# Kernel optimization log

Measured on AMD Instinct MI355X. Metric: run time of the kernel, lower is better.

The kernel has to match this reference:

```python
import jax, jax.numpy as jnp
import numpy as np

N_NODES = 500000
N_EDGES = 8000000


def gcn_conv(x, W, b, src, dst, n_nodes):
    # PyG GCNConv: add self-loops, symmetric normalization, x@W, scatter-add.
    loop = jnp.arange(n_nodes, dtype=src.dtype)
    src_a = jnp.concatenate([src, loop])  # [E+N]
    dst_a = jnp.concatenate([dst, loop])
    deg = jax.ops.segment_sum(jnp.ones_like(dst_a, dtype=x.dtype), dst_a,
                              num_segments=n_nodes)  # in-degree incl. self-loop
    dinv = jnp.where(deg > 0, jax.lax.rsqrt(deg), 0.0)
    norm = dinv[src_a] * dinv[dst_a]  # [E+N]
    xw = x @ W  # [N, out]
    msg = xw[src_a] * norm[:, None]  # [E+N, out]
    out = jax.ops.segment_sum(msg, dst_a, num_segments=n_nodes)
    return out + b


def setup_inputs() -> dict:
    key = jax.random.key(0)
    k1, k2, k3, k4, k5, k6 = jax.random.split(key, 6)
    x = jax.random.uniform(k1, (N_NODES, 1), dtype=jnp.float32)
    edge_index = jax.random.randint(k2, (2, N_EDGES), 0, N_NODES, dtype=jnp.int32)
    W1 = jax.random.normal(k3, (1, 16), dtype=jnp.float32)
    b1 = jax.random.normal(k4, (16,), dtype=jnp.float32) * 0.1
    W2 = jax.random.normal(k5, (16, 2), dtype=jnp.float32)
    b2 = jax.random.normal(k6, (2,), dtype=jnp.float32) * 0.1
    return {"x": x, "edge_index": edge_index, "W1": W1, "b1": b1,
            "W2": W2, "b2": b2}


def reference(x, edge_index, W1, b1, W2, b2):
    src, dst = edge_index[0], edge_index[1]
    h = gcn_conv(x, W1, b1, src, dst, N_NODES)
    h = jax.nn.relu(h)
    # dropout is identity in eval mode
    h = gcn_conv(h, W2, b2, src, dst, N_NODES)
    return jax.nn.log_softmax(h, axis=1)
```

## Files before the change

### kernel.cpp

```cpp
#include <hip/hip_runtime.h>
#include <math.h>


typedef unsigned int uint4v __attribute__((ext_vector_type(4)));

#define NPB 1024
#define NPB_SHIFT 10
#define NPB_MASK (NPB - 1)
#define MAXB 512
#define P1T 512
#define CHUNK 16384
#define SORT_CAP 17408
#define SPT 17

__device__ __forceinline__ unsigned short f2bf(float f) {
    unsigned int x = __float_as_uint(f);
    x += 0x7fffu + ((x >> 16) & 1u);
    return (unsigned short)(x >> 16);
}
__device__ __forceinline__ float bf2f(unsigned short h) {
    return __uint_as_float((unsigned int)h << 16);
}

__global__ __launch_bounds__(P1T, 4) void k_bucket(
    const int* __restrict__ src, const int* __restrict__ dst,
    unsigned int* __restrict__ file, int* __restrict__ ctr,
    int E, int nbucket, int cap)
{
    __shared__ unsigned int sorted[CHUNK];
    __shared__ int cnt[MAXB];
    __shared__ int pre[MAXB + 1];
    __shared__ int gb[MAXB];
    __shared__ int rk[MAXB];

    const int t  = threadIdx.x;
    const int e0 = blockIdx.x * CHUNK;
    const int nE = min(CHUNK, E - e0);

    for (int b = t; b < MAXB; b += P1T) { cnt[b] = 0; rk[b] = 0; }
    __syncthreads();

    const bool full = (nE == CHUNK);
    int4 dc[8];

    if (full) {
        const int4* d4 = (const int4*)(dst + e0);
#pragma unroll
        for (int k = 0; k < 8; ++k) dc[k] = d4[t + k * P1T];
#pragma unroll
        for (int k = 0; k < 8; ++k) {
            atomicAdd(&cnt[((unsigned)dc[k].x) >> NPB_SHIFT], 1);
            atomicAdd(&cnt[((unsigned)dc[k].y) >> NPB_SHIFT], 1);
            atomicAdd(&cnt[((unsigned)dc[k].z) >> NPB_SHIFT], 1);
            atomicAdd(&cnt[((unsigned)dc[k].w) >> NPB_SHIFT], 1);
        }
    } else {
        for (int i = t; i < nE; i += P1T)
            atomicAdd(&cnt[((unsigned)dst[e0 + i]) >> NPB_SHIFT], 1);
    }
    __syncthreads();

    int v = (t < nbucket) ? cnt[t] : 0;
    pre[t + 1] = v;
    if (t == 0) pre[0] = 0;
    __syncthreads();
    for (int off = 1; off < P1T; off <<= 1) {
        int add = (t >= off) ? pre[t + 1 - off] : 0;
        __syncthreads();
        pre[t + 1] += add;
        __syncthreads();
    }

    for (int b = t; b < nbucket; b += P1T) {
        int c = cnt[b];
        gb[b] = c ? atomicAdd(&ctr[b], c) : 0;
    }
    __syncthreads();

    if (full) {
        const int4* s4 = (const int4*)(src + e0);
#pragma unroll
        for (int k = 0; k < 8; ++k) {
            int4 s = s4[t + k * P1T];
            int4 d = dc[k];
            {
                int b = ((unsigned)d.x) >> NPB_SHIFT;
                int r = atomicAdd(&rk[b], 1);
                sorted[pre[b] + r] = (((unsigned)s.x) << NPB_SHIFT) | ((unsigned)d.x & NPB_MASK);
            }
            {
                int b = ((unsigned)d.y) >> NPB_SHIFT;
                int r = atomicAdd(&rk[b], 1);
                sorted[pre[b] + r] = (((unsigned)s.y) << NPB_SHIFT) | ((unsigned)d.y & NPB_MASK);
            }
            {
                int b = ((unsigned)d.z) >> NPB_SHIFT;
                int r = atomicAdd(&rk[b], 1);
                sorted[pre[b] + r] = (((unsigned)s.z) << NPB_SHIFT) | ((unsigned)d.z & NPB_MASK);
            }
            {
                int b = ((unsigned)d.w) >> NPB_SHIFT;
                int r = atomicAdd(&rk[b], 1);
                sorted[pre[b] + r] = (((unsigned)s.w) << NPB_SHIFT) | ((unsigned)d.w & NPB_MASK);
            }
        }
    } else {
        for (int i = t; i < nE; i += P1T) {
            int d = dst[e0 + i];
            int b = ((unsigned)d) >> NPB_SHIFT;
            unsigned int w = (((unsigned)src[e0 + i]) << NPB_SHIFT) |
                             ((unsigned)d & NPB_MASK);
            int r = atomicAdd(&rk[b], 1);
            sorted[pre[b] + r] = w;
        }
    }
    __syncthreads();

    {
        const int wid  = t >> 6;
        const int lane = t & 63;
        const int nw   = P1T >> 6;
        for (int b = wid; b < nbucket; b += nw) {
            int s0 = pre[b], s1 = pre[b + 1];
            int base = gb[b];
            unsigned int* dp = file + (size_t)b * cap;
            for (int j = s0 + lane; j < s1; j += 64) {
                int idx = base + (j - s0);
                if (idx < cap)
                    __builtin_nontemporal_store(sorted[j], &dp[idx]);
            }
        }
    }
}

__global__ __launch_bounds__(NPB) void k_sort(
    unsigned int* __restrict__ file, const int* __restrict__ ctr,
    int* __restrict__ start, const float* __restrict__ x,
    float* __restrict__ dinv, unsigned short* __restrict__ u,
    int N, int cap)
{
    __shared__ unsigned int sorted[SORT_CAP];
    __shared__ int cnt[NPB];
    __shared__ int pre[NPB + 1];

    const int t = threadIdx.x;
    const int b = blockIdx.x;
    const int nb = min(ctr[b], cap);
    unsigned int* f = file + (size_t)b * cap;

    cnt[t] = 0;
    __syncthreads();

    unsigned int ev[SPT];
    int rk_[SPT];
#pragma unroll
    for (int k = 0; k < SPT; ++k) {
        int i = t + (k << NPB_SHIFT);
        if (i < nb) ev[k] = __builtin_nontemporal_load(f + i);
    }
#pragma unroll
    for (int k = 0; k < SPT; ++k) {
        int i = t + (k << NPB_SHIFT);
        if (i < nb) rk_[k] = atomicAdd(&cnt[ev[k] & NPB_MASK], 1);
    }
    __syncthreads();

    pre[t + 1] = cnt[t];
    if (t == 0) pre[0] = 0;
    __syncthreads();
    for (int off = 1; off < NPB; off <<= 1) {
        int add = (t >= off) ? pre[t + 1 - off] : 0;
        __syncthreads();
        pre[t + 1] += add;
        __syncthreads();
    }

#pragma unroll
    for (int k = 0; k < SPT; ++k) {
        int i = t + (k << NPB_SHIFT);
        if (i < nb)
            sorted[pre[ev[k] & NPB_MASK] + rk_[k]] = ev[k] >> NPB_SHIFT;
    }
    __syncthreads();

    for (int i = t; i < nb; i += NPB)
        __builtin_nontemporal_store(sorted[i], &f[i]);

    start[b * (NPB + 1) + t] = pre[t];
    if (t == 0) start[b * (NPB + 1) + NPB] = pre[NPB];

    const int g = b * NPB + t;
    if (g < N) {
        float dv = rsqrtf((float)(cnt[t] + 1));
        dinv[g] = dv;
        u[g] = f2bf(x[g] * dv);
    }
}

__global__ __launch_bounds__(256) void k_agg1(
    const unsigned int* __restrict__ file, const int* __restrict__ start,
    const unsigned short* __restrict__ u, const float* __restrict__ dinv,
    const float* __restrict__ W1, const float* __restrict__ b1,
    const float* __restrict__ W2, unsigned int* __restrict__ q,
    int N, int cap)
{
    int g = blockIdx.x * 256 + threadIdx.x;
    if (g >= N) return;
    int b = g >> NPB_SHIFT, loc = g & NPB_MASK;
    const int* st = start + b * (NPB + 1);
    int e0 = st[loc], e1 = st[loc + 1];
    const unsigned int* f = file + (size_t)b * cap;

    float acc = 0.f;
    int j = e0;
    for (; j + 4 <= e1; j += 4) {
        unsigned int s0 = f[j], s1 = f[j + 1], s2 = f[j + 2], s3 = f[j + 3];
        float a = bf2f(u[s0]), bb = bf2f(u[s1]);
        float c = bf2f(u[s2]), d = bf2f(u[s3]);
        acc += (a + bb) + (c + d);
    }
    for (; j < e1; ++j) acc += bf2f(u[f[j]]);

    float dv = dinv[g];
    float s1v = (acc + bf2f(u[g])) * dv;
    float c0 = 0.f, c1 = 0.f;
#pragma unroll
    for (int k = 0; k < 16; ++k) {
        float h = fmaxf(fmaf(s1v, W1[k], b1[k]), 0.f);
        c0 = fmaf(h, W2[2 * k], c0);
        c1 = fmaf(h, W2[2 * k + 1], c1);
    }
    q[g] = (unsigned int)f2bf(c0 * dv) | ((unsigned int)f2bf(c1 * dv) << 16);
}

__global__ __launch_bounds__(256) void k_agg2(
    const unsigned int* __restrict__ file, const int* __restrict__ start,
    const unsigned int* __restrict__ q, const float* __restrict__ dinv,
    const float* __restrict__ b2, float2* __restrict__ out,
    int N, int cap)
{
    int g = blockIdx.x * 256 + threadIdx.x;
    if (g >= N) return;
    int b = g >> NPB_SHIFT, loc = g & NPB_MASK;
    const int* st = start + b * (NPB + 1);
    int e0 = st[loc], e1 = st[loc + 1];
    const unsigned int* f = file + (size_t)b * cap;

    float a0 = 0.f, a1 = 0.f;
    int j = e0;
    for (; j + 4 <= e1; j += 4) {
        unsigned int g0 = q[f[j]], g1 = q[f[j + 1]];
        unsigned int g2 = q[f[j + 2]], g3 = q[f[j + 3]];
        a0 += (bf2f((unsigned short)g0) + bf2f((unsigned short)g1)) +
              (bf2f((unsigned short)g2) + bf2f((unsigned short)g3));
        a1 += (bf2f((unsigned short)(g0 >> 16)) + bf2f((unsigned short)(g1 >> 16))) +
              (bf2f((unsigned short)(g2 >> 16)) + bf2f((unsigned short)(g3 >> 16)));
    }
    for (; j < e1; ++j) {
        unsigned int gq = q[f[j]];
        a0 += bf2f((unsigned short)gq);
        a1 += bf2f((unsigned short)(gq >> 16));
    }

    float dv = dinv[g];
    unsigned int qi = q[g];
    float o0 = (a0 + bf2f((unsigned short)qi)) * dv + b2[0];
    float o1 = (a1 + bf2f((unsigned short)(qi >> 16))) * dv + b2[1];
    float m = fmaxf(o0, o1);
    float l = m + logf(expf(o0 - m) + expf(o1 - m));
    out[g] = make_float2(o0 - l, o1 - l);
}

#define NT 256
__global__ __launch_bounds__(NT) void fb_deg(const int* __restrict__ dst,
                                             int* __restrict__ deg, int E) {
    int e = blockIdx.x * blockDim.x + threadIdx.x;
    if (e < E) atomicAdd(&deg[dst[e]], 1);
}
__global__ __launch_bounds__(NT) void fb_node1(const float* __restrict__ x,
                                               const int* __restrict__ deg,
                                               float* __restrict__ dinv,
                                               float* __restrict__ u, int N) {
    int i = blockIdx.x * blockDim.x + threadIdx.x;
    if (i < N) {
        float dv = rsqrtf((float)(deg[i] + 1));
        dinv[i] = dv;
        u[i] = x[i] * dv;
    }
}
__global__ __launch_bounds__(NT) void fb_edge1(const int* __restrict__ src,
                                               const int* __restrict__ dst,
                                               const float* __restrict__ u,
                                               float* __restrict__ agg1, int E) {
    int e = blockIdx.x * blockDim.x + threadIdx.x;
    if (e < E) atomicAdd(&agg1[dst[e]], u[src[e]]);
}
__global__ __launch_bounds__(NT) void fb_node2(const float* __restrict__ agg1,
                                               const float* __restrict__ u,
                                               const float* __restrict__ dinv,
                                               const float* __restrict__ W1,
                                               const float* __restrict__ b1,
                                               const float* __restrict__ W2,
                                               float2* __restrict__ q, int N) {
    int i = blockIdx.x * blockDim.x + threadIdx.x;
    if (i < N) {
        float dv = dinv[i];
        float s1 = (agg1[i] + u[i]) * dv;
        float c0 = 0.f, c1 = 0.f;
#pragma unroll
        for (int k = 0; k < 16; ++k) {
            float h = fmaxf(fmaf(s1, W1[k], b1[k]), 0.f);
            c0 = fmaf(h, W2[2 * k], c0);
            c1 = fmaf(h, W2[2 * k + 1], c1);
        }
        q[i] = make_float2(c0 * dv, c1 * dv);
    }
}
__global__ __launch_bounds__(NT) void fb_edge2(const int* __restrict__ src,
                                               const int* __restrict__ dst,
                                               const float2* __restrict__ q,
                                               float* __restrict__ agg2, int E) {
    int e = blockIdx.x * blockDim.x + threadIdx.x;
    if (e < E) {
        float2 qq = q[src[e]];
        atomicAdd(&agg2[2 * dst[e]], qq.x);
        atomicAdd(&agg2[2 * dst[e] + 1], qq.y);
    }
}
__global__ __launch_bounds__(NT) void fb_node3(const float* __restrict__ agg2,
                                               const float2* __restrict__ q,
                                               const float* __restrict__ dinv,
                                               const float* __restrict__ b2,
                                               float2* __restrict__ out, int N) {
    int i = blockIdx.x * blockDim.x + threadIdx.x;
    if (i < N) {
        float dv = dinv[i];
        float2 qi = q[i];
        float o0 = (agg2[2 * i] + qi.x) * dv + b2[0];
        float o1 = (agg2[2 * i + 1] + qi.y) * dv + b2[1];
        float m = fmaxf(o0, o1);
        float l = m + logf(expf(o0 - m) + expf(o1 - m));
        out[i] = make_float2(o0 - l, o1 - l);
    }
}

extern "C" void kernel_launch(void* const* d_in, const int* in_sizes, int n_in,
                              void* d_out, int out_size, void* d_ws, size_t ws_size,
                              hipStream_t stream) {
    const float* x  = (const float*)d_in[0];
    const int* ei   = (const int*)d_in[1];
    const float* W1 = (const float*)d_in[2];
    const float* b1 = (const float*)d_in[3];
    const float* W2 = (const float*)d_in[4];
    const float* b2 = (const float*)d_in[5];

    const int N = in_sizes[0];
    const int E = in_sizes[1] / 2;
    const int* src = ei;
    const int* dst = ei + E;

    const int nbucket = (N + NPB - 1) / NPB;
    const int cap = ((E / nbucket + 1024) + 63) & ~63;

    auto align_up = [](size_t v) { return (v + 255) & ~(size_t)255; };
    size_t off_ctr   = 0;
    size_t off_file  = align_up((size_t)MAXB * sizeof(int));
    size_t off_start = align_up(off_file + (size_t)nbucket * SORT_CAP * sizeof(unsigned int));
    size_t off_dinv  = align_up(off_start + (size_t)nbucket * (NPB + 1) * sizeof(int));
    size_t off_u     = align_up(off_dinv + (size_t)N * sizeof(float));
    size_t off_q     = align_up(off_u + (size_t)N * sizeof(unsigned short));
    size_t needed    = off_q + (size_t)N * sizeof(unsigned int);

    char* ws = (char*)d_ws;

    if (nbucket <= MAXB && cap <= SORT_CAP && needed <= ws_size) {
        int*            ctr   = (int*)(ws + off_ctr);
        unsigned int*   file  = (unsigned int*)(ws + off_file);
        int*            start = (int*)(ws + off_start);
        float*          dinv  = (float*)(ws + off_dinv);
        unsigned short* u     = (unsigned short*)(ws + off_u);
        unsigned int*   q     = (unsigned int*)(ws + off_q);

        (void)hipMemsetAsync(ctr, 0, (size_t)MAXB * sizeof(int), stream);

        const int p1Blocks  = (E + CHUNK - 1) / CHUNK;
        const int nodBlocks = (N + 255) / 256;
        k_bucket<<<p1Blocks, P1T, 0, stream>>>(src, dst, file, ctr, E, nbucket, SORT_CAP);
        k_sort  <<<nbucket, NPB, 0, stream>>>(file, ctr, start, x, dinv, u, N, SORT_CAP);
        k_agg1  <<<nodBlocks, 256, 0, stream>>>(file, start, u, dinv, W1, b1, W2, q, N, SORT_CAP);
        k_agg2  <<<nodBlocks, 256, 0, stream>>>(file, start, q, dinv, b2, (float2*)d_out, N, SORT_CAP);
    } else {
        int*    deg  = (int*)   (ws);
        float*  agg1 = (float*) (ws + (size_t)4 * N);
        float*  agg2 = (float*) (ws + (size_t)8 * N);
        float*  dinv = (float*) (ws + (size_t)16 * N);
        float*  u    = (float*) (ws + (size_t)20 * N);
        float2* q    = (float2*)(ws + (size_t)24 * N);
        (void)hipMemsetAsync(ws, 0, (size_t)16 * N, stream);
        const int nodeBlocks = (N + NT - 1) / NT;
        const int edgeBlocks = (E + NT - 1) / NT;
        fb_deg  <<<edgeBlocks, NT, 0, stream>>>(dst, deg, E);
        fb_node1<<<nodeBlocks, NT, 0, stream>>>(x, deg, dinv, u, N);
        fb_edge1<<<edgeBlocks, NT, 0, stream>>>(src, dst, u, agg1, E);
        fb_node2<<<nodeBlocks, NT, 0, stream>>>(agg1, u, dinv, W1, b1, W2, q, N);
        fb_edge2<<<edgeBlocks, NT, 0, stream>>>(src, dst, q, agg2, E);
        fb_node3<<<nodeBlocks, NT, 0, stream>>>(agg2, q, dinv, b2, (float2*)d_out, N);
    }
}
```

Baseline: 237.8 us.

## Use 16 lanes per node in aggregation kernels and shuffle-based block scans

The two aggregation kernels now assign 16 lanes to each destination node instead of one thread. The lanes stride over the node's CSR edge list with coalesced nontemporal loads, reduce through shuffles, and pass the sum via shared memory to a finishing step. This removes divergence and serial gather chains from variable degrees (about 16 edges per node on average) in exchange for more threads, a block barrier and idle lanes. Separately, the Hillis-Steele shared-memory prefix scans in the bucket and sort kernels become wave-level shuffle scans, cutting the number of barriers.

```diff
diff --git a/kernel.cpp b/kernel.cpp
--- a/kernel.cpp
+++ b/kernel.cpp
@@ -12,6 +12,9 @@
 #define CHUNK 16384
 #define SORT_CAP 17408
 #define SPT 17
+#define AGG_T 1024
+#define LPN 16
+#define NPBK (AGG_T / LPN)
 
 __device__ __forceinline__ unsigned short f2bf(float f) {
     unsigned int x = __float_as_uint(f);
@@ -32,6 +35,7 @@
     __shared__ int pre[MAXB + 1];
     __shared__ int gb[MAXB];
     __shared__ int rk[MAXB];
+    __shared__ int wsum[P1T / 64];
 
     const int t  = threadIdx.x;
     const int e0 = blockIdx.x * CHUNK;
@@ -60,16 +64,30 @@
     }
     __syncthreads();
 
-    int v = (t < nbucket) ? cnt[t] : 0;
-    pre[t + 1] = v;
-    if (t == 0) pre[0] = 0;
-    __syncthreads();
-    for (int off = 1; off < P1T; off <<= 1) {
-        int add = (t >= off) ? pre[t + 1 - off] : 0;
+    {
+        const int lane = t & 63, wv = t >> 6;
+        int v = (t < nbucket) ? cnt[t] : 0;
+#pragma unroll
+        for (int d = 1; d < 64; d <<= 1) {
+            int nv = __shfl_up(v, d, 64);
+            if (lane >= d) v += nv;
+        }
+        if (lane == 63) wsum[wv] = v;
         __syncthreads();
-        pre[t + 1] += add;
+        if (t < P1T / 64) {
+            int s = wsum[t];
+#pragma unroll
+            for (int d = 1; d < P1T / 64; d <<= 1) {
+                int ns = __shfl_up(s, d, P1T / 64);
+                if (t >= d) s += ns;
+            }
+            wsum[t] = s;
+        }
         __syncthreads();
-    }
+        pre[t + 1] = (wv ? wsum[wv - 1] : 0) + v;
+        if (t == 0) pre[0] = 0;
+    }
+    __syncthreads();
 
     for (int b = t; b < nbucket; b += P1T) {
         int c = cnt[b];
@@ -142,6 +160,7 @@
     __shared__ unsigned int sorted[SORT_CAP];
     __shared__ int cnt[NPB];
     __shared__ int pre[NPB + 1];
+    __shared__ int wsum[NPB / 64];
 
     const int t = threadIdx.x;
     const int b = blockIdx.x;
@@ -165,15 +184,30 @@
     }
     __syncthreads();
 
-    pre[t + 1] = cnt[t];
-    if (t == 0) pre[0] = 0;
-    __syncthreads();
-    for (int off = 1; off < NPB; off <<= 1) {
-        int add = (t >= off) ? pre[t + 1 - off] : 0;
+    {
+        const int lane = t & 63, wv = t >> 6;
+        int v = cnt[t];
+#pragma unroll
+        for (int d = 1; d < 64; d <<= 1) {
+            int nv = __shfl_up(v, d, 64);
+            if (lane >= d) v += nv;
+        }
+        if (lane == 63) wsum[wv] = v;
         __syncthreads();
-        pre[t + 1] += add;
+        if (t < NPB / 64) {
+            int s = wsum[t];
+#pragma unroll
+            for (int d = 1; d < NPB / 64; d <<= 1) {
+                int ns = __shfl_up(s, d, NPB / 64);
+                if (t >= d) s += ns;
+            }
+            wsum[t] = s;
+        }
         __syncthreads();
-    }
+        pre[t + 1] = (wv ? wsum[wv - 1] : 0) + v;
+        if (t == 0) pre[0] = 0;
+    }
+    __syncthreads();
 
 #pragma unroll
     for (int k = 0; k < SPT; ++k) {
@@ -197,78 +231,96 @@
     }
 }
 
-__global__ __launch_bounds__(256) void k_agg1(
+__global__ __launch_bounds__(AGG_T) void k_agg1(
     const unsigned int* __restrict__ file, const int* __restrict__ start,
     const unsigned short* __restrict__ u, const float* __restrict__ dinv,
     const float* __restrict__ W1, const float* __restrict__ b1,
     const float* __restrict__ W2, unsigned int* __restrict__ q,
     int N, int cap)
 {
-    int g = blockIdx.x * 256 + threadIdx.x;
-    if (g >= N) return;
-    int b = g >> NPB_SHIFT, loc = g & NPB_MASK;
-    const int* st = start + b * (NPB + 1);
-    int e0 = st[loc], e1 = st[loc + 1];
-    const unsigned int* f = file + (size_t)b * cap;
+    __shared__ float sacc[NPBK];
+    const int t = threadIdx.x;
+    const int grp = t >> 4;
+    const int sl  = t & (LPN - 1);
+    const int g = blockIdx.x * NPBK + grp;
 
     float acc = 0.f;
-    int j = e0;
-    for (; j + 4 <= e1; j += 4) {
-        unsigned int s0 = f[j], s1 = f[j + 1], s2 = f[j + 2], s3 = f[j + 3];
-        float a = bf2f(u[s0]), bb = bf2f(u[s1]);
-        float c = bf2f(u[s2]), d = bf2f(u[s3]);
-        acc += (a + bb) + (c + d);
-    }
-    for (; j < e1; ++j) acc += bf2f(u[f[j]]);
-
-    float dv = dinv[g];
-    float s1v = (acc + bf2f(u[g])) * dv;
-    float c0 = 0.f, c1 = 0.f;
-#pragma unroll
-    for (int k = 0; k < 16; ++k) {
-        float h = fmaxf(fmaf(s1v, W1[k], b1[k]), 0.f);
-        c0 = fmaf(h, W2[2 * k], c0);
-        c1 = fmaf(h, W2[2 * k + 1], c1);
-    }
-    q[g] = (unsigned int)f2bf(c0 * dv) | ((unsigned int)f2bf(c1 * dv) << 16);
-}
-
-__global__ __launch_bounds__(256) void k_agg2(
+    if (g < N) {
+        int b = g >> NPB_SHIFT, loc = g & NPB_MASK;
+        const int* st = start + b * (NPB + 1);
+        int e0 = st[loc], e1 = st[loc + 1];
+        const unsigned int* f = file + (size_t)b * cap;
+        for (int j = e0 + sl; j < e1; j += LPN)
+            acc += bf2f(u[__builtin_nontemporal_load(f + j)]);
+    }
+#pragma unroll
+    for (int d = LPN / 2; d; d >>= 1) acc += __shfl_down(acc, d, LPN);
+    if (sl == 0) sacc[grp] = acc;
+    __syncthreads();
+
+    if (t < NPBK) {
+        int g2 = blockIdx.x * NPBK + t;
+        if (g2 < N) {
+            float dv = dinv[g2];
+            float s1v = (sacc[t] + bf2f(u[g2])) * dv;
+            float c0 = 0.f, c1 = 0.f;
+#pragma unroll
+            for (int k = 0; k < 16; ++k) {
+                float h = fmaxf(fmaf(s1v, W1[k], b1[k]), 0.f);
+                c0 = fmaf(h, W2[2 * k], c0);
+                c1 = fmaf(h, W2[2 * k + 1], c1);
+            }
+            q[g2] = (unsigned int)f2bf(c0 * dv) |
+                    ((unsigned int)f2bf(c1 * dv) << 16);
+        }
+    }
+}
+
+__global__ __launch_bounds__(AGG_T) void k_agg2(
     const unsigned int* __restrict__ file, const int* __restrict__ start,
     const unsigned int* __restrict__ q, const float* __restrict__ dinv,
     const float* __restrict__ b2, float2* __restrict__ out,
     int N, int cap)
 {
-    int g = blockIdx.x * 256 + threadIdx.x;
-    if (g >= N) return;
-    int b = g >> NPB_SHIFT, loc = g & NPB_MASK;
-    const int* st = start + b * (NPB + 1);
-    int e0 = st[loc], e1 = st[loc + 1];
-    const unsigned int* f = file + (size_t)b * cap;
+    __shared__ float s0a[NPBK];
+    __shared__ float s1a[NPBK];
+    const int t = threadIdx.x;
+    const int grp = t >> 4;
+    const int sl  = t & (LPN - 1);
+    const int g = blockIdx.x * NPBK + grp;
 
     float a0 = 0.f, a1 = 0.f;
-    int j = e0;
-    for (; j + 4 <= e1; j += 4) {
-        unsigned int g0 = q[f[j]], g1 = q[f[j + 1]];
-        unsigned int g2 = q[f[j + 2]], g3 = q[f[j + 3]];
-        a0 += (bf2f((unsigned short)g0) + bf2f((unsigned short)g1)) +
-              (bf2f((unsigned short)g2) + bf2f((unsigned short)g3));
-        a1 += (bf2f((unsigned short)(g0 >> 16)) + bf2f((unsigned short)(g1 >> 16))) +
-              (bf2f((unsigned short)(g2 >> 16)) + bf2f((unsigned short)(g3 >> 16)));
-    }
-    for (; j < e1; ++j) {
-        unsigned int gq = q[f[j]];
-        a0 += bf2f((unsigned short)gq);
-        a1 += bf2f((unsigned short)(gq >> 16));
-    }
-
-    float dv = dinv[g];
-    unsigned int qi = q[g];
-    float o0 = (a0 + bf2f((unsigned short)qi)) * dv + b2[0];
-    float o1 = (a1 + bf2f((unsigned short)(qi >> 16))) * dv + b2[1];
-    float m = fmaxf(o0, o1);
-    float l = m + logf(expf(o0 - m) + expf(o1 - m));
-    out[g] = make_float2(o0 - l, o1 - l);
+    if (g < N) {
+        int b = g >> NPB_SHIFT, loc = g & NPB_MASK;
+        const int* st = start + b * (NPB + 1);
+        int e0 = st[loc], e1 = st[loc + 1];
+        const unsigned int* f = file + (size_t)b * cap;
+        for (int j = e0 + sl; j < e1; j += LPN) {
+            unsigned int gq = q[__builtin_nontemporal_load(f + j)];
+            a0 += bf2f((unsigned short)gq);
+            a1 += bf2f((unsigned short)(gq >> 16));
+        }
+    }
+#pragma unroll
+    for (int d = LPN / 2; d; d >>= 1) {
+        a0 += __shfl_down(a0, d, LPN);
+        a1 += __shfl_down(a1, d, LPN);
+    }
+    if (sl == 0) { s0a[grp] = a0; s1a[grp] = a1; }
+    __syncthreads();
+
+    if (t < NPBK) {
+        int g2 = blockIdx.x * NPBK + t;
+        if (g2 < N) {
+            float dv = dinv[g2];
+            unsigned int qi = q[g2];
+            float o0 = (s0a[t] + bf2f((unsigned short)qi)) * dv + b2[0];
+            float o1 = (s1a[t] + bf2f((unsigned short)(qi >> 16))) * dv + b2[1];
+            float m = fmaxf(o0, o1);
+            float l = m + logf(expf(o0 - m) + expf(o1 - m));
+            out[g2] = make_float2(o0 - l, o1 - l);
+        }
+    }
 }
 
 #define NT 256
@@ -384,11 +436,11 @@
         (void)hipMemsetAsync(ctr, 0, (size_t)MAXB * sizeof(int), stream);
 
         const int p1Blocks  = (E + CHUNK - 1) / CHUNK;
-        const int nodBlocks = (N + 255) / 256;
+        const int aggBlocks = (N + NPBK - 1) / NPBK;
         k_bucket<<<p1Blocks, P1T, 0, stream>>>(src, dst, file, ctr, E, nbucket, SORT_CAP);
         k_sort  <<<nbucket, NPB, 0, stream>>>(file, ctr, start, x, dinv, u, N, SORT_CAP);
-        k_agg1  <<<nodBlocks, 256, 0, stream>>>(file, start, u, dinv, W1, b1, W2, q, N, SORT_CAP);
-        k_agg2  <<<nodBlocks, 256, 0, stream>>>(file, start, q, dinv, b2, (float2*)d_out, N, SORT_CAP);
+        k_agg1  <<<aggBlocks, AGG_T, 0, stream>>>(file, start, u, dinv, W1, b1, W2, q, N, SORT_CAP);
+        k_agg2  <<<aggBlocks, AGG_T, 0, stream>>>(file, start, q, dinv, b2, (float2*)d_out, N, SORT_CAP);
     } else {
         int*    deg  = (int*)   (ws);
         float*  agg1 = (float*) (ws + (size_t)4 * N);
```

Result: slower. 271.1 us (+14.0%).

## Reuse histogram atomics as ranks, use wave-shuffle scans, and vectorize aligned edge loads

Applied to the files above, without the earlier changes.

In the bucketing kernel, the first-pass atomicAdd results are kept as per-edge ranks, so the second pass of shared-memory atomics goes away. The cnt array is dropped and the occupancy hint is removed from launch_bounds. Both the bucket and sort kernels replace the barrier-heavy Hillis-Steele shared-memory scan with a two-level wavefront shuffle scan. The aggregation kernels read aligned runs of edge indices as 128-bit nontemporal vector loads, with scalar head and tail loops. The cost is 32 extra rank registers per thread in k_bucket, which can lower occupancy.

```diff
diff --git a/kernel.cpp b/kernel.cpp
--- a/kernel.cpp
+++ b/kernel.cpp
@@ -10,8 +10,11 @@
 #define MAXB 512
 #define P1T 512
 #define CHUNK 16384
+#define EPT 32
 #define SORT_CAP 17408
 #define SPT 17
+
+#define NTL4(p) __builtin_nontemporal_load((const uint4v*)(p))
 
 __device__ __forceinline__ unsigned short f2bf(float f) {
     unsigned int x = __float_as_uint(f);
@@ -22,26 +25,27 @@
     return __uint_as_float((unsigned int)h << 16);
 }
 
-__global__ __launch_bounds__(P1T, 4) void k_bucket(
+__global__ __launch_bounds__(P1T) void k_bucket(
     const int* __restrict__ src, const int* __restrict__ dst,
     unsigned int* __restrict__ file, int* __restrict__ ctr,
     int E, int nbucket, int cap)
 {
     __shared__ unsigned int sorted[CHUNK];
-    __shared__ int cnt[MAXB];
+    __shared__ int rk[MAXB];
     __shared__ int pre[MAXB + 1];
     __shared__ int gb[MAXB];
-    __shared__ int rk[MAXB];
+    __shared__ int wsum[P1T / 64];
 
     const int t  = threadIdx.x;
     const int e0 = blockIdx.x * CHUNK;
     const int nE = min(CHUNK, E - e0);
 
-    for (int b = t; b < MAXB; b += P1T) { cnt[b] = 0; rk[b] = 0; }
+    for (int b = t; b < MAXB; b += P1T) rk[b] = 0;
     __syncthreads();
 
     const bool full = (nE == CHUNK);
     int4 dc[8];
+    int  rnk[EPT];
 
     if (full) {
         const int4* d4 = (const int4*)(dst + e0);
@@ -49,30 +53,45 @@
         for (int k = 0; k < 8; ++k) dc[k] = d4[t + k * P1T];
 #pragma unroll
         for (int k = 0; k < 8; ++k) {
-            atomicAdd(&cnt[((unsigned)dc[k].x) >> NPB_SHIFT], 1);
-            atomicAdd(&cnt[((unsigned)dc[k].y) >> NPB_SHIFT], 1);
-            atomicAdd(&cnt[((unsigned)dc[k].z) >> NPB_SHIFT], 1);
-            atomicAdd(&cnt[((unsigned)dc[k].w) >> NPB_SHIFT], 1);
+            rnk[4 * k]     = atomicAdd(&rk[((unsigned)dc[k].x) >> NPB_SHIFT], 1);
+            rnk[4 * k + 1] = atomicAdd(&rk[((unsigned)dc[k].y) >> NPB_SHIFT], 1);
+            rnk[4 * k + 2] = atomicAdd(&rk[((unsigned)dc[k].z) >> NPB_SHIFT], 1);
+            rnk[4 * k + 3] = atomicAdd(&rk[((unsigned)dc[k].w) >> NPB_SHIFT], 1);
         }
     } else {
-        for (int i = t; i < nE; i += P1T)
-            atomicAdd(&cnt[((unsigned)dst[e0 + i]) >> NPB_SHIFT], 1);
-    }
-    __syncthreads();
-
-    int v = (t < nbucket) ? cnt[t] : 0;
-    pre[t + 1] = v;
-    if (t == 0) pre[0] = 0;
-    __syncthreads();
-    for (int off = 1; off < P1T; off <<= 1) {
-        int add = (t >= off) ? pre[t + 1 - off] : 0;
+        int k = 0;
+        for (int i = t; i < nE; i += P1T, ++k)
+            rnk[k] = atomicAdd(&rk[((unsigned)dst[e0 + i]) >> NPB_SHIFT], 1);
+    }
+    __syncthreads();
+
+    {
+        const int lane = t & 63, wv = t >> 6;
+        int v = (t < nbucket) ? rk[t] : 0;
+#pragma unroll
+        for (int d = 1; d < 64; d <<= 1) {
+            int nv = __shfl_up(v, d, 64);
+            if (lane >= d) v += nv;
+        }
+        if (lane == 63) wsum[wv] = v;
         __syncthreads();
-        pre[t + 1] += add;
+        if (t < P1T / 64) {
+            int s = wsum[t];
+#pragma unroll
+            for (int d = 1; d < P1T / 64; d <<= 1) {
+                int ns = __shfl_up(s, d, P1T / 64);
+                if (t >= d) s += ns;
+            }
+            wsum[t] = s;
+        }
         __syncthreads();
-    }
+        pre[t + 1] = (wv ? wsum[wv - 1] : 0) + v;
+        if (t == 0) pre[0] = 0;
+    }
+    __syncthreads();
 
     for (int b = t; b < nbucket; b += P1T) {
-        int c = cnt[b];
+        int c = pre[b + 1] - pre[b];
         gb[b] = c ? atomicAdd(&ctr[b], c) : 0;
     }
     __syncthreads();
@@ -83,35 +102,22 @@
         for (int k = 0; k < 8; ++k) {
             int4 s = s4[t + k * P1T];
             int4 d = dc[k];
-            {
-                int b = ((unsigned)d.x) >> NPB_SHIFT;
-                int r = atomicAdd(&rk[b], 1);
-                sorted[pre[b] + r] = (((unsigned)s.x) << NPB_SHIFT) | ((unsigned)d.x & NPB_MASK);
-            }
-            {
-                int b = ((unsigned)d.y) >> NPB_SHIFT;
-                int r = atomicAdd(&rk[b], 1);
-                sorted[pre[b] + r] = (((unsigned)s.y) << NPB_SHIFT) | ((unsigned)d.y & NPB_MASK);
-            }
-            {
-                int b = ((unsigned)d.z) >> NPB_SHIFT;
-                int r = atomicAdd(&rk[b], 1);
-                sorted[pre[b] + r] = (((unsigned)s.z) << NPB_SHIFT) | ((unsigned)d.z & NPB_MASK);
-            }
-            {
-                int b = ((unsigned)d.w) >> NPB_SHIFT;
-                int r = atomicAdd(&rk[b], 1);
-                sorted[pre[b] + r] = (((unsigned)s.w) << NPB_SHIFT) | ((unsigned)d.w & NPB_MASK);
-            }
+            sorted[pre[((unsigned)d.x) >> NPB_SHIFT] + rnk[4 * k]] =
+                (((unsigned)s.x) << NPB_SHIFT) | ((unsigned)d.x & NPB_MASK);
+            sorted[pre[((unsigned)d.y) >> NPB_SHIFT] + rnk[4 * k + 1]] =
+                (((unsigned)s.y) << NPB_SHIFT) | ((unsigned)d.y & NPB_MASK);
+            sorted[pre[((unsigned)d.z) >> NPB_SHIFT] + rnk[4 * k + 2]] =
+                (((unsigned)s.z) << NPB_SHIFT) | ((unsigned)d.z & NPB_MASK);
+            sorted[pre[((unsigned)d.w) >> NPB_SHIFT] + rnk[4 * k + 3]] =
+                (((unsigned)s.w) << NPB_SHIFT) | ((unsigned)d.w & NPB_MASK);
         }
     } else {
-        for (int i = t; i < nE; i += P1T) {
+        int k = 0;
+        for (int i = t; i < nE; i += P1T, ++k) {
             int d = dst[e0 + i];
             int b = ((unsigned)d) >> NPB_SHIFT;
-            unsigned int w = (((unsigned)src[e0 + i]) << NPB_SHIFT) |
-                             ((unsigned)d & NPB_MASK);
-            int r = atomicAdd(&rk[b], 1);
-            sorted[pre[b] + r] = w;
+            sorted[pre[b] + rnk[k]] =
+                (((unsigned)src[e0 + i]) << NPB_SHIFT) | ((unsigned)d & NPB_MASK);
         }
     }
     __syncthreads();
@@ -142,6 +148,7 @@
     __shared__ unsigned int sorted[SORT_CAP];
     __shared__ int cnt[NPB];
     __shared__ int pre[NPB + 1];
+    __shared__ int wsum[NPB / 64];
 
     const int t = threadIdx.x;
     const int b = blockIdx.x;
@@ -165,15 +172,30 @@
     }
     __syncthreads();
 
-    pre[t + 1] = cnt[t];
-    if (t == 0) pre[0] = 0;
-    __syncthreads();
-    for (int off = 1; off < NPB; off <<= 1) {
-        int add = (t >= off) ? pre[t + 1 - off] : 0;
+    {
+        const int lane = t & 63, wv = t >> 6;
+        int v = cnt[t];
+#pragma unroll
+        for (int d = 1; d < 64; d <<= 1) {
+            int nv = __shfl_up(v, d, 64);
+            if (lane >= d) v += nv;
+        }
+        if (lane == 63) wsum[wv] = v;
         __syncthreads();
-        pre[t + 1] += add;
+        if (t < NPB / 64) {
+            int s = wsum[t];
+#pragma unroll
+            for (int d = 1; d < NPB / 64; d <<= 1) {
+                int ns = __shfl_up(s, d, NPB / 64);
+                if (t >= d) s += ns;
+            }
+            wsum[t] = s;
+        }
         __syncthreads();
-    }
+        pre[t + 1] = (wv ? wsum[wv - 1] : 0) + v;
+        if (t == 0) pre[0] = 0;
+    }
+    __syncthreads();
 
 #pragma unroll
     for (int k = 0; k < SPT; ++k) {
@@ -213,13 +235,17 @@
 
     float acc = 0.f;
     int j = e0;
-    for (; j + 4 <= e1; j += 4) {
-        unsigned int s0 = f[j], s1 = f[j + 1], s2 = f[j + 2], s3 = f[j + 3];
-        float a = bf2f(u[s0]), bb = bf2f(u[s1]);
-        float c = bf2f(u[s2]), d = bf2f(u[s3]);
-        acc += (a + bb) + (c + d);
-    }
-    for (; j < e1; ++j) acc += bf2f(u[f[j]]);
+    int ja = (e0 + 3) & ~3;
+    int jb = e1 & ~3;
+    if (ja > jb) ja = e1;
+    for (; j < ja; ++j) acc += bf2f(u[__builtin_nontemporal_load(f + j)]);
+    for (; j < jb; j += 4) {
+        uint4v w = NTL4(f + j);
+        float v0 = bf2f(u[w.x]), v1 = bf2f(u[w.y]);
+        float v2 = bf2f(u[w.z]), v3 = bf2f(u[w.w]);
+        acc += (v0 + v1) + (v2 + v3);
+    }
+    for (; j < e1; ++j) acc += bf2f(u[__builtin_nontemporal_load(f + j)]);
 
     float dv = dinv[g];
     float s1v = (acc + bf2f(u[g])) * dv;
@@ -248,16 +274,24 @@
 
     float a0 = 0.f, a1 = 0.f;
     int j = e0;
-    for (; j + 4 <= e1; j += 4) {
-        unsigned int g0 = q[f[j]], g1 = q[f[j + 1]];
-        unsigned int g2 = q[f[j + 2]], g3 = q[f[j + 3]];
+    int ja = (e0 + 3) & ~3;
+    int jb = e1 & ~3;
+    if (ja > jb) ja = e1;
+    for (; j < ja; ++j) {
+        unsigned int gq = q[__builtin_nontemporal_load(f + j)];
+        a0 += bf2f((unsigned short)gq);
+        a1 += bf2f((unsigned short)(gq >> 16));
+    }
+    for (; j < jb; j += 4) {
+        uint4v w = NTL4(f + j);
+        unsigned int g0 = q[w.x], g1 = q[w.y], g2 = q[w.z], g3 = q[w.w];
         a0 += (bf2f((unsigned short)g0) + bf2f((unsigned short)g1)) +
               (bf2f((unsigned short)g2) + bf2f((unsigned short)g3));
         a1 += (bf2f((unsigned short)(g0 >> 16)) + bf2f((unsigned short)(g1 >> 16))) +
               (bf2f((unsigned short)(g2 >> 16)) + bf2f((unsigned short)(g3 >> 16)));
     }
     for (; j < e1; ++j) {
-        unsigned int gq = q[f[j]];
+        unsigned int gq = q[__builtin_nontemporal_load(f + j)];
         a0 += bf2f((unsigned short)gq);
         a1 += bf2f((unsigned short)(gq >> 16));
     }
```

Result: slower. 286.4 us (+20.4%).
